# Kernel tuning notes

Hardware: AMD Instinct MI355X
Metric: run time of the kernel (lower is better)

## Reference

```python
import jax, jax.numpy as jnp
import numpy as np

S_IN, S_OUT = 64, 128
NX, NS, CIN, COUT = 40000, 200000, 128, 64


def _unique_coords(key, n, S):
    lin = jax.random.permutation(key, S ** 3)[:n]
    return jnp.stack([lin // (S * S), (lin // S) % S, lin % S], axis=-1).astype(jnp.int32)


def setup_inputs() -> dict:
    key = jax.random.key(0)
    ks = jax.random.split(key, 8)
    cords = _unique_coords(ks[0], NX, S_IN)          # unique low-res coords
    skip_cords = _unique_coords(ks[1], NS, S_OUT)    # unique high-res coords
    x_feats = jax.random.normal(ks[2], (NX, CIN), jnp.float32)
    skip_feats = jax.random.normal(ks[3], (NS, COUT), jnp.float32)
    w_up = jax.random.normal(ks[4], (8, CIN, COUT), jnp.float32) * 0.05
    w1 = jax.random.normal(ks[5], (27, COUT, COUT), jnp.float32) * 0.05
    w2 = jax.random.normal(ks[6], (27, COUT, COUT), jnp.float32) * 0.05
    w3 = jax.random.normal(ks[7], (27, COUT, COUT), jnp.float32) * 0.05
    ones = jnp.ones((COUT,), jnp.float32)
    zeros = jnp.zeros((COUT,), jnp.float32)
    return dict(x_feats=x_feats, skip_feats=skip_feats, w_up=w_up, w1=w1, w2=w2, w3=w3,
                g1=ones, b1=zeros, g2=ones, b2=zeros, g3=ones, b3=zeros,
                cords=cords, skip_cords=skip_cords, spatial_size=64)


def _lin(c, S):
    return (c[..., 0] * S + c[..., 1]) * S + c[..., 2]


def _bn(f, g, b):
    # BatchNorm1d, batch stats (track_running_stats=False), eps=1e-4, biased var
    mu = f.mean(axis=0)
    var = f.var(axis=0)
    return (f - mu) * jax.lax.rsqrt(var + 1e-4) * g + b


def _lrelu(z, s):
    return jnp.where(z >= 0, z, s * z)


def reference(x_feats, skip_feats, w_up, w1, w2, w3, g1, b1, g2, b2, g3, b3,
              cords, skip_cords, spatial_size):
    S = 2 * int(spatial_size)  # output spatial size after upsample
    Cout = w_up.shape[-1]
    # --- upsample: each active voxel c emits a 2x2x2 block at 2c+o, weight W[1-o] ---
    offs8 = jnp.stack(jnp.meshgrid(*([jnp.arange(2)] * 3), indexing='ij'), -1).reshape(8, 3).astype(jnp.int32)
    out_cords = ((2 * cords)[:, None, :] + offs8[None, :, :]).reshape(-1, 3)        # [8N,3]
    feats = jnp.einsum('nc,ocd->nod', x_feats, w_up[::-1]).reshape(-1, Cout)         # [8N,C]
    M = feats.shape[0]
    lin_out = _lin(out_cords, S)
    # --- sparse_add: hash-match skip coords, add matched skip features ---
    table_s = jnp.full((S ** 3,), -1, jnp.int32).at[_lin(skip_cords, S)].set(
        jnp.arange(skip_cords.shape[0], dtype=jnp.int32))
    j = table_s[lin_out]
    feats = feats + jnp.where((j >= 0)[:, None], skip_feats[jnp.clip(j, 0)], 0.0)
    # --- neighbor table for 3x3x3 submanifold convs over the fixed active set ---
    table_o = jnp.full((S ** 3,), -1, jnp.int32).at[lin_out].set(jnp.arange(M, dtype=jnp.int32))
    offs27 = jnp.stack(jnp.meshgrid(*([jnp.arange(-1, 2)] * 3), indexing='ij'), -1).reshape(27, 3).astype(jnp.int32)
    nb = out_cords[None, :, :] + offs27[:, None, :]                                  # [27,M,3]
    valid = jnp.all((nb >= 0) & (nb < S), axis=-1)
    lin_nb = jnp.where(valid, _lin(nb, S), 0)
    nbr = jnp.where(valid, table_o[lin_nb], -1)                                      # [27,M]

    def subconv(f, W):
        acc = jnp.zeros((M, W.shape[-1]), f.dtype)
        for k in range(27):  # fixed small kernel loop
            idx = nbr[k]
            m = (idx >= 0).astype(f.dtype)[:, None]
            acc = acc + (f[jnp.clip(idx, 0)] * m) @ W[k]
        return acc

    x1 = _lrelu(_bn(subconv(feats, w1), g1, b1), 0.05)
    x2 = _lrelu(_bn(subconv(x1, w2), g2, b2), 0.05)
    x3 = _bn(subconv(x2, w3), g3, b3)
    return _lrelu(x3 + x1, 0.333)
```

## Files before the change

kernel.cpp:

```cpp
#include <hip/hip_runtime.h>


#define S2 128
#define TABN (S2 * S2 * S2)

typedef __attribute__((ext_vector_type(8))) short short8;
typedef __attribute__((ext_vector_type(4))) float f32x4;

__device__ inline float b2f(unsigned short u) {
    return __uint_as_float(((unsigned)u) << 16);
}
__device__ inline unsigned short f2b(float f) {
    unsigned u = __float_as_uint(f);
    return (unsigned short)((u + 0x7FFF + ((u >> 16) & 1)) >> 16);
}

__global__ void k_scatter_skip(const int* __restrict__ sc, int* __restrict__ table_s, int NS) {
    int i = blockIdx.x * 256 + threadIdx.x;
    if (i >= NS) return;
    table_s[(sc[i * 3] * S2 + sc[i * 3 + 1]) * S2 + sc[i * 3 + 2]] = i;
}

__global__ void k_packw(const float* __restrict__ w, unsigned short* __restrict__ wpk) {
    int t = blockIdx.x * 256 + threadIdx.x;
    if (t >= 27 * 4096) return;
    int j = t & 7, l = (t >> 3) & 63, nt = (t >> 9) & 3, ks = (t >> 11) & 1, k = t >> 12;
    int d = ks * 32 + (l >> 4) * 8 + j;
    int c = nt * 16 + (l & 15);
    wpk[t] = f2b(w[(k * 64 + d) * 64 + c]);
}

__global__ __launch_bounds__(256) void k_upsample(
    const float* __restrict__ x, const float* __restrict__ wup,
    const int* __restrict__ cords, const float* __restrict__ skipf,
    const int* __restrict__ table_s, int* __restrict__ table_o,
    unsigned short* __restrict__ feats, int NX) {
    __shared__ float xl[16][132];
    int tid = threadIdx.x;
    int P0 = blockIdx.x * 16;
    {
        int p = tid >> 4, d0 = (tid & 15) * 8;
        const float* src = x + (size_t)(P0 + p) * 128 + d0;
        float4 a = *(const float4*)src;
        float4 b = *(const float4*)(src + 4);
        xl[p][d0 + 0] = a.x; xl[p][d0 + 1] = a.y; xl[p][d0 + 2] = a.z; xl[p][d0 + 3] = a.w;
        xl[p][d0 + 4] = b.x; xl[p][d0 + 5] = b.y; xl[p][d0 + 6] = b.z; xl[p][d0 + 7] = b.w;
    }
    __syncthreads();
    int c = tid & 63, g = tid >> 6;
    float acc[8][4];
#pragma unroll
    for (int o = 0; o < 8; ++o)
#pragma unroll
        for (int p = 0; p < 4; ++p) acc[o][p] = 0.f;
    for (int d = 0; d < 128; ++d) {
        float xv0 = xl[g * 4 + 0][d], xv1 = xl[g * 4 + 1][d];
        float xv2 = xl[g * 4 + 2][d], xv3 = xl[g * 4 + 3][d];
#pragma unroll
        for (int o = 0; o < 8; ++o) {
            float wv = wup[(size_t)(7 - o) * 8192 + d * 64 + c];
            acc[o][0] += xv0 * wv; acc[o][1] += xv1 * wv;
            acc[o][2] += xv2 * wv; acc[o][3] += xv3 * wv;
        }
    }
    for (int p = 0; p < 4; ++p) {
        int parent = P0 + g * 4 + p;
        int cx = cords[parent * 3], cy = cords[parent * 3 + 1], cz = cords[parent * 3 + 2];
#pragma unroll
        for (int o = 0; o < 8; ++o) {
            int X = 2 * cx + (o >> 2), Y = 2 * cy + ((o >> 1) & 1), Z = 2 * cz + (o & 1);
            int lin = (X * S2 + Y) * S2 + Z;
            int m = parent * 8 + o;
            int j = table_s[lin];
            float v = acc[o][p];
            if (j >= 0) v += skipf[(size_t)j * 64 + c];
            feats[(size_t)m * 64 + c] = f2b(v);
            if (c == 0) table_o[lin] = m;
        }
    }
}

__global__ void k_build_nbr(const int* __restrict__ cords, const int* __restrict__ table_o,
                            int* __restrict__ nbr, int M) {
    int m = blockIdx.x * 256 + threadIdx.x;
    if (m >= M) return;
    int n = m >> 3, o = m & 7;
    int X = 2 * cords[n * 3] + (o >> 2);
    int Y = 2 * cords[n * 3 + 1] + ((o >> 1) & 1);
    int Z = 2 * cords[n * 3 + 2] + (o & 1);
#pragma unroll
    for (int kk = 0; kk < 27; ++kk) {
        int nx = X + kk / 9 - 1, ny = Y + (kk / 3) % 3 - 1, nz = Z + kk % 3 - 1;
        int idx = -1;
        if ((unsigned)nx < (unsigned)S2 && (unsigned)ny < (unsigned)S2 && (unsigned)nz < (unsigned)S2)
            idx = table_o[(nx * S2 + ny) * S2 + nz];
        nbr[(size_t)kk * M + m] = idx;
    }
}

__global__ __launch_bounds__(256) void k_conv_mfma(
    const unsigned short* __restrict__ fin, const unsigned short* __restrict__ wpk,
    const int* __restrict__ nbr, unsigned short* __restrict__ zout,
    float* __restrict__ stats, int M) {
    int tid = threadIdx.x;
    int lane = tid & 63, wv = tid >> 6;
    int l15 = lane & 15, kg = lane >> 4;
    int rbase = blockIdx.x * 128 + wv * 32;

    f32x4 acc[2][4];
#pragma unroll
    for (int m = 0; m < 2; ++m)
#pragma unroll
        for (int nt = 0; nt < 4; ++nt) acc[m][nt] = (f32x4){0.f, 0.f, 0.f, 0.f};

    const short8 kzero = {0, 0, 0, 0, 0, 0, 0, 0};
    for (int k = 0; k < 27; ++k) {
        const int* nrow = nbr + (size_t)k * M + rbase;
        int i0 = nrow[l15];
        int i1 = nrow[16 + l15];
        const unsigned short* p0 = fin + (size_t)(i0 < 0 ? 0 : i0) * 64 + kg * 8;
        const unsigned short* p1 = fin + (size_t)(i1 < 0 ? 0 : i1) * 64 + kg * 8;
        short8 a00 = *(const short8*)p0;
        short8 a01 = *(const short8*)(p0 + 32);
        short8 a10 = *(const short8*)p1;
        short8 a11 = *(const short8*)(p1 + 32);
        if (i0 < 0) { a00 = kzero; a01 = kzero; }
        if (i1 < 0) { a10 = kzero; a11 = kzero; }
        const unsigned short* wb = wpk + (size_t)k * 4096 + lane * 8;
#pragma unroll
        for (int nt = 0; nt < 4; ++nt) {
            short8 b0 = *(const short8*)(wb + nt * 512);
            short8 b1 = *(const short8*)(wb + 2048 + nt * 512);
            acc[0][nt] = __builtin_amdgcn_mfma_f32_16x16x32_bf16(a00, b0, acc[0][nt], 0, 0, 0);
            acc[0][nt] = __builtin_amdgcn_mfma_f32_16x16x32_bf16(a01, b1, acc[0][nt], 0, 0, 0);
            acc[1][nt] = __builtin_amdgcn_mfma_f32_16x16x32_bf16(a10, b0, acc[1][nt], 0, 0, 0);
            acc[1][nt] = __builtin_amdgcn_mfma_f32_16x16x32_bf16(a11, b1, acc[1][nt], 0, 0, 0);
        }
    }

    float s[4] = {0.f, 0.f, 0.f, 0.f}, q[4] = {0.f, 0.f, 0.f, 0.f};
#pragma unroll
    for (int m = 0; m < 2; ++m)
#pragma unroll
        for (int nt = 0; nt < 4; ++nt)
#pragma unroll
            for (int j = 0; j < 4; ++j) {
                float v = acc[m][nt][j];
                int row = rbase + m * 16 + kg * 4 + j;
                zout[(size_t)row * 64 + nt * 16 + l15] = f2b(v);
                s[nt] += v; q[nt] += v * v;
            }
#pragma unroll
    for (int nt = 0; nt < 4; ++nt) {
        float ss = s[nt], qq = q[nt];
        ss += __shfl_xor(ss, 16); ss += __shfl_xor(ss, 32);
        qq += __shfl_xor(qq, 16); qq += __shfl_xor(qq, 32);
        if (kg == 0) {
            atomicAdd(&stats[nt * 16 + l15], ss);
            atomicAdd(&stats[64 + nt * 16 + l15], qq);
        }
    }
}

__global__ void k_finalize(const float* __restrict__ stats, const float* __restrict__ g,
                           const float* __restrict__ b, float* __restrict__ coef, float invM) {
    int c = threadIdx.x;
    if (c >= 64) return;
    float mu = stats[c] * invM;
    float var = stats[64 + c] * invM - mu * mu;
    float sc = g[c] * rsqrtf(var + 1e-4f);
    coef[c] = sc;
    coef[64 + c] = b[c] - mu * sc;
}

__global__ void k_xform(unsigned short* __restrict__ z, const float* __restrict__ coef, int n8) {
    int t = blockIdx.x * 256 + threadIdx.x;
    if (t >= n8) return;
    short8 v = ((const short8*)z)[t];
    int cb = (t * 8) & 63;
    short8 r;
#pragma unroll
    for (int j = 0; j < 8; ++j) {
        float f = b2f((unsigned short)v[j]) * coef[cb + j] + coef[64 + cb + j];
        f = fmaxf(f, 0.05f * f);
        r[j] = (short)f2b(f);
    }
    ((short8*)z)[t] = r;
}

__global__ void k_final(const unsigned short* __restrict__ z3,
                        const unsigned short* __restrict__ x1,
                        const float* __restrict__ coef3, float* __restrict__ out, int n8) {
    int t = blockIdx.x * 256 + threadIdx.x;
    if (t >= n8) return;
    short8 v3 = ((const short8*)z3)[t];
    short8 v1 = ((const short8*)x1)[t];
    int cb = (t * 8) & 63;
    float4 o0, o1;
    float rr[8];
#pragma unroll
    for (int j = 0; j < 8; ++j) {
        float f3 = b2f((unsigned short)v3[j]) * coef3[cb + j] + coef3[64 + cb + j];
        float r = f3 + b2f((unsigned short)v1[j]);
        rr[j] = fmaxf(r, 0.333f * r);
    }
    o0 = make_float4(rr[0], rr[1], rr[2], rr[3]);
    o1 = make_float4(rr[4], rr[5], rr[6], rr[7]);
    ((float4*)out)[t * 2] = o0;
    ((float4*)out)[t * 2 + 1] = o1;
}

extern "C" void kernel_launch(void* const* d_in, const int* in_sizes, int n_in,
                              void* d_out, int out_size, void* d_ws, size_t ws_size,
                              hipStream_t stream) {
    const float* x_feats    = (const float*)d_in[0];
    const float* skip_feats = (const float*)d_in[1];
    const float* w_up       = (const float*)d_in[2];
    const float* w1         = (const float*)d_in[3];
    const float* w2         = (const float*)d_in[4];
    const float* w3         = (const float*)d_in[5];
    const float* g1 = (const float*)d_in[6],  *b1 = (const float*)d_in[7];
    const float* g2 = (const float*)d_in[8],  *b2 = (const float*)d_in[9];
    const float* g3 = (const float*)d_in[10], *b3 = (const float*)d_in[11];
    const int* cords      = (const int*)d_in[12];
    const int* skip_cords = (const int*)d_in[13];
    int NX = in_sizes[12] / 3;
    int NS = in_sizes[13] / 3;
    int M = NX * 8;

    char* ws = (char*)d_ws;
    size_t off = 0;
    auto alloc = [&](size_t bytes) -> char* {
        char* p = ws + off;
        off += (bytes + 255) & ~(size_t)255;
        return p;
    };
    int* table_s = (int*)alloc((size_t)TABN * 4);
    int* table_o = (int*)alloc((size_t)TABN * 4);
    int* nbr     = (int*)alloc((size_t)27 * M * 4);
    unsigned short* A = (unsigned short*)alloc((size_t)M * 64 * 2);
    unsigned short* B = (unsigned short*)alloc((size_t)M * 64 * 2);
    unsigned short* C = (unsigned short*)alloc((size_t)M * 64 * 2);
    unsigned short* wp1 = (unsigned short*)alloc(27 * 4096 * 2);
    unsigned short* wp2 = (unsigned short*)alloc(27 * 4096 * 2);
    unsigned short* wp3 = (unsigned short*)alloc(27 * 4096 * 2);
    float* stats = (float*)alloc(384 * 4);
    float* coefs = (float*)alloc(384 * 4);

    hipMemsetAsync(table_s, 0xFF, (size_t)TABN * 4, stream);
    hipMemsetAsync(table_o, 0xFF, (size_t)TABN * 4, stream);
    hipMemsetAsync(stats, 0, 384 * 4, stream);

    float invM = 1.f / (float)M;
    int n8 = M * 64 / 8;

    k_scatter_skip<<<(NS + 255) / 256, 256, 0, stream>>>(skip_cords, table_s, NS);
    k_packw<<<432, 256, 0, stream>>>(w1, wp1);
    k_packw<<<432, 256, 0, stream>>>(w2, wp2);
    k_packw<<<432, 256, 0, stream>>>(w3, wp3);
    k_upsample<<<NX / 16, 256, 0, stream>>>(x_feats, w_up, cords, skip_feats,
                                            table_s, table_o, A, NX);
    k_build_nbr<<<(M + 255) / 256, 256, 0, stream>>>(cords, table_o, nbr, M);

    k_conv_mfma<<<M / 128, 256, 0, stream>>>(A, wp1, nbr, B, stats, M);
    k_finalize<<<1, 64, 0, stream>>>(stats, g1, b1, coefs, invM);
    k_xform<<<(n8 + 255) / 256, 256, 0, stream>>>(B, coefs, n8);

    k_conv_mfma<<<M / 128, 256, 0, stream>>>(B, wp2, nbr, C, stats + 128, M);
    k_finalize<<<1, 64, 0, stream>>>(stats + 128, g2, b2, coefs + 128, invM);
    k_xform<<<(n8 + 255) / 256, 256, 0, stream>>>(C, coefs + 128, n8);

    k_conv_mfma<<<M / 128, 256, 0, stream>>>(C, wp3, nbr, A, stats + 256, M);
    k_finalize<<<1, 64, 0, stream>>>(stats + 256, g3, b3, coefs + 256, invM);

    k_final<<<(n8 + 255) / 256, 256, 0, stream>>>(A, B, coefs + 256, (float*)d_out, n8);
}
```

Baseline: 1.370 ms.

## Move upsample to bf16 MFMA and software-pipeline conv gathers with LDS neighbor indices

The upsample GEMM now runs on bf16 MFMA, using a pre-converted bf16 copy of x and pre-packed upsample weights, in place of scalar FP32 FMAs. The subconv kernel stages the block's neighbor indices in LDS and software-pipelines the gathered A and B loads two steps ahead of the MFMAs. Missing neighbors now point to an extra zero row at index M, which removes the per-load masking, and launch bounds request two blocks per CU. This adds conversion and packing kernels and raises register pressure, and the upsample input is rounded to bf16, which changes precision.

After: 1.227 ms. 10.4% less time.

```diff
diff --git a/kernel.cpp b/kernel.cpp
--- a/kernel.cpp
+++ b/kernel.cpp
@@ -13,6 +13,17 @@
 __device__ inline unsigned short f2b(float f) {
     unsigned u = __float_as_uint(f);
     return (unsigned short)((u + 0x7FFF + ((u >> 16) & 1)) >> 16);
+}
+
+__global__ void k_cvt(const float* __restrict__ x, unsigned short* __restrict__ xb, int n8) {
+    int t = blockIdx.x * 256 + threadIdx.x;
+    if (t >= n8) return;
+    float4 a = ((const float4*)x)[t * 2];
+    float4 b = ((const float4*)x)[t * 2 + 1];
+    short8 r;
+    r[0] = (short)f2b(a.x); r[1] = (short)f2b(a.y); r[2] = (short)f2b(a.z); r[3] = (short)f2b(a.w);
+    r[4] = (short)f2b(b.x); r[5] = (short)f2b(b.y); r[6] = (short)f2b(b.z); r[7] = (short)f2b(b.w);
+    ((short8*)xb)[t] = r;
 }
 
 __global__ void k_scatter_skip(const int* __restrict__ sc, int* __restrict__ table_s, int NS) {
@@ -30,52 +41,57 @@
     wpk[t] = f2b(w[(k * 64 + d) * 64 + c]);
 }
 
-__global__ __launch_bounds__(256) void k_upsample(
-    const float* __restrict__ x, const float* __restrict__ wup,
+__global__ void k_packwup(const float* __restrict__ w, unsigned short* __restrict__ wpku) {
+    int t = blockIdx.x * 256 + threadIdx.x;
+    if (t >= 65536) return;
+    int j = t & 7, l = (t >> 3) & 63, nt = (t >> 9) & 31, ks = t >> 14;
+    int d = ks * 32 + (l >> 4) * 8 + j;
+    int col = nt * 16 + (l & 15);
+    int o = col >> 6, c = col & 63;
+    wpku[t] = f2b(w[(size_t)(7 - o) * 8192 + d * 64 + c]);
+}
+
+__global__ __launch_bounds__(256) void k_upsample_mfma(
+    const unsigned short* __restrict__ xb, const unsigned short* __restrict__ wpku,
     const int* __restrict__ cords, const float* __restrict__ skipf,
     const int* __restrict__ table_s, int* __restrict__ table_o,
     unsigned short* __restrict__ feats, int NX) {
-    __shared__ float xl[16][132];
     int tid = threadIdx.x;
-    int P0 = blockIdx.x * 16;
-    {
-        int p = tid >> 4, d0 = (tid & 15) * 8;
-        const float* src = x + (size_t)(P0 + p) * 128 + d0;
-        float4 a = *(const float4*)src;
-        float4 b = *(const float4*)(src + 4);
-        xl[p][d0 + 0] = a.x; xl[p][d0 + 1] = a.y; xl[p][d0 + 2] = a.z; xl[p][d0 + 3] = a.w;
-        xl[p][d0 + 4] = b.x; xl[p][d0 + 5] = b.y; xl[p][d0 + 6] = b.z; xl[p][d0 + 7] = b.w;
-    }
-    __syncthreads();
-    int c = tid & 63, g = tid >> 6;
-    float acc[8][4];
-#pragma unroll
-    for (int o = 0; o < 8; ++o)
-#pragma unroll
-        for (int p = 0; p < 4; ++p) acc[o][p] = 0.f;
-    for (int d = 0; d < 128; ++d) {
-        float xv0 = xl[g * 4 + 0][d], xv1 = xl[g * 4 + 1][d];
-        float xv2 = xl[g * 4 + 2][d], xv3 = xl[g * 4 + 3][d];
-#pragma unroll
-        for (int o = 0; o < 8; ++o) {
-            float wv = wup[(size_t)(7 - o) * 8192 + d * 64 + c];
-            acc[o][0] += xv0 * wv; acc[o][1] += xv1 * wv;
-            acc[o][2] += xv2 * wv; acc[o][3] += xv3 * wv;
+    int lane = tid & 63, w = tid >> 6;
+    int l15 = lane & 15, kg = lane >> 4;
+    int p0 = blockIdx.x * 16;
+
+    f32x4 acc[8];
+#pragma unroll
+    for (int nt = 0; nt < 8; ++nt) acc[nt] = (f32x4){0.f, 0.f, 0.f, 0.f};
+
+#pragma unroll
+    for (int ks = 0; ks < 4; ++ks) {
+        short8 a = *(const short8*)(xb + (size_t)(p0 + l15) * 128 + ks * 32 + kg * 8);
+        const unsigned short* wb = wpku + ((size_t)(ks * 32 + w * 8) * 64 + lane) * 8;
+#pragma unroll
+        for (int nt = 0; nt < 8; ++nt) {
+            short8 b = *(const short8*)(wb + nt * 512);
+            acc[nt] = __builtin_amdgcn_mfma_f32_16x16x32_bf16(a, b, acc[nt], 0, 0, 0);
         }
     }
-    for (int p = 0; p < 4; ++p) {
-        int parent = P0 + g * 4 + p;
+
+#pragma unroll
+    for (int j = 0; j < 4; ++j) {
+        int parent = p0 + kg * 4 + j;
         int cx = cords[parent * 3], cy = cords[parent * 3 + 1], cz = cords[parent * 3 + 2];
 #pragma unroll
-        for (int o = 0; o < 8; ++o) {
+        for (int nt = 0; nt < 8; ++nt) {
+            int o = w * 2 + (nt >> 2);
+            int c = (nt & 3) * 16 + l15;
             int X = 2 * cx + (o >> 2), Y = 2 * cy + ((o >> 1) & 1), Z = 2 * cz + (o & 1);
             int lin = (X * S2 + Y) * S2 + Z;
-            int m = parent * 8 + o;
-            int j = table_s[lin];
-            float v = acc[o][p];
-            if (j >= 0) v += skipf[(size_t)j * 64 + c];
-            feats[(size_t)m * 64 + c] = f2b(v);
-            if (c == 0) table_o[lin] = m;
+            int row = parent * 8 + o;
+            int js = table_s[lin];
+            float v = acc[nt][j];
+            if (js >= 0) v += skipf[(size_t)js * 64 + c];
+            feats[(size_t)row * 64 + c] = f2b(v);
+            if (c == 0) table_o[lin] = row;
         }
     }
 }
@@ -94,18 +110,31 @@
         int idx = -1;
         if ((unsigned)nx < (unsigned)S2 && (unsigned)ny < (unsigned)S2 && (unsigned)nz < (unsigned)S2)
             idx = table_o[(nx * S2 + ny) * S2 + nz];
-        nbr[(size_t)kk * M + m] = idx;
-    }
-}
-
-__global__ __launch_bounds__(256) void k_conv_mfma(
+        nbr[(size_t)kk * M + m] = (idx < 0) ? M : idx;
+    }
+}
+
+__global__ __launch_bounds__(256, 2) void k_conv_mfma(
     const unsigned short* __restrict__ fin, const unsigned short* __restrict__ wpk,
     const int* __restrict__ nbr, unsigned short* __restrict__ zout,
     float* __restrict__ stats, int M) {
+    __shared__ int idx_lds[32 * 128];
     int tid = threadIdx.x;
     int lane = tid & 63, wv = tid >> 6;
     int l15 = lane & 15, kg = lane >> 4;
-    int rbase = blockIdx.x * 128 + wv * 32;
+    int rblk = blockIdx.x * 128;
+    int rw = wv * 32;
+
+    {
+        int col = (tid & 31) * 4;
+        int q0 = tid >> 5;
+        for (int q = q0; q < 27; q += 8) {
+            int4 v = *(const int4*)(nbr + (size_t)q * M + rblk + col);
+            *(int4*)&idx_lds[q * 128 + col] = v;
+        }
+        for (int i = tid; i < 5 * 128; i += 256) idx_lds[27 * 128 + i] = M;
+    }
+    __syncthreads();
 
     f32x4 acc[2][4];
 #pragma unroll
@@ -113,30 +142,51 @@
 #pragma unroll
         for (int nt = 0; nt < 4; ++nt) acc[m][nt] = (f32x4){0.f, 0.f, 0.f, 0.f};
 
-    const short8 kzero = {0, 0, 0, 0, 0, 0, 0, 0};
-    for (int k = 0; k < 27; ++k) {
-        const int* nrow = nbr + (size_t)k * M + rbase;
-        int i0 = nrow[l15];
-        int i1 = nrow[16 + l15];
-        const unsigned short* p0 = fin + (size_t)(i0 < 0 ? 0 : i0) * 64 + kg * 8;
-        const unsigned short* p1 = fin + (size_t)(i1 < 0 ? 0 : i1) * 64 + kg * 8;
-        short8 a00 = *(const short8*)p0;
-        short8 a01 = *(const short8*)(p0 + 32);
-        short8 a10 = *(const short8*)p1;
-        short8 a11 = *(const short8*)(p1 + 32);
-        if (i0 < 0) { a00 = kzero; a01 = kzero; }
-        if (i1 < 0) { a10 = kzero; a11 = kzero; }
-        const unsigned short* wb = wpk + (size_t)k * 4096 + lane * 8;
-#pragma unroll
-        for (int nt = 0; nt < 4; ++nt) {
-            short8 b0 = *(const short8*)(wb + nt * 512);
-            short8 b1 = *(const short8*)(wb + 2048 + nt * 512);
-            acc[0][nt] = __builtin_amdgcn_mfma_f32_16x16x32_bf16(a00, b0, acc[0][nt], 0, 0, 0);
-            acc[0][nt] = __builtin_amdgcn_mfma_f32_16x16x32_bf16(a01, b1, acc[0][nt], 0, 0, 0);
-            acc[1][nt] = __builtin_amdgcn_mfma_f32_16x16x32_bf16(a10, b0, acc[1][nt], 0, 0, 0);
-            acc[1][nt] = __builtin_amdgcn_mfma_f32_16x16x32_bf16(a11, b1, acc[1][nt], 0, 0, 0);
-        }
-    }
+    short8 A0[2][2], A1[2][2], A2[2][2], A3[2][2], B0[2][4], B1[2][4];
+
+#define LOADA(Ab, kk)                                                          \
+    {                                                                          \
+        _Pragma("unroll")                                                      \
+        for (int m = 0; m < 2; ++m) {                                          \
+            int idx = idx_lds[(kk) * 128 + rw + m * 16 + l15];                 \
+            const unsigned short* p = fin + (size_t)idx * 64 + kg * 8;         \
+            Ab[m][0] = *(const short8*)p;                                      \
+            Ab[m][1] = *(const short8*)(p + 32);                               \
+        }                                                                      \
+    }
+#define LOADB(Bb, kk)                                                          \
+    {                                                                          \
+        int kb = (kk) > 26 ? 26 : (kk);                                        \
+        const unsigned short* wb = wpk + (size_t)kb * 4096 + lane * 8;         \
+        _Pragma("unroll")                                                      \
+        for (int ks = 0; ks < 2; ++ks)                                         \
+            _Pragma("unroll")                                                  \
+            for (int nt = 0; nt < 4; ++nt)                                     \
+                Bb[ks][nt] = *(const short8*)(wb + ks * 2048 + nt * 512);      \
+    }
+#define MFMAQ(Ab, Bb)                                                          \
+    {                                                                          \
+        _Pragma("unroll")                                                      \
+        for (int m = 0; m < 2; ++m)                                            \
+            _Pragma("unroll")                                                  \
+            for (int nt = 0; nt < 4; ++nt) {                                   \
+                acc[m][nt] = __builtin_amdgcn_mfma_f32_16x16x32_bf16(          \
+                    Ab[m][0], Bb[0][nt], acc[m][nt], 0, 0, 0);                 \
+                acc[m][nt] = __builtin_amdgcn_mfma_f32_16x16x32_bf16(          \
+                    Ab[m][1], Bb[1][nt], acc[m][nt], 0, 0, 0);                 \
+            }                                                                  \
+    }
+
+    LOADA(A0, 0); LOADA(A1, 1); LOADB(B0, 0);
+    for (int k = 0; k < 28; k += 4) {
+        LOADA(A2, k + 2); LOADB(B1, k + 1); MFMAQ(A0, B0);
+        LOADA(A3, k + 3); LOADB(B0, k + 2); MFMAQ(A1, B1);
+        LOADA(A0, k + 4); LOADB(B1, k + 3); MFMAQ(A2, B0);
+        LOADA(A1, k + 5); LOADB(B0, k + 4); MFMAQ(A3, B1);
+    }
+#undef LOADA
+#undef LOADB
+#undef MFMAQ
 
     float s[4] = {0.f, 0.f, 0.f, 0.f}, q[4] = {0.f, 0.f, 0.f, 0.f};
 #pragma unroll
@@ -146,7 +196,7 @@
 #pragma unroll
             for (int j = 0; j < 4; ++j) {
                 float v = acc[m][nt][j];
-                int row = rbase + m * 16 + kg * 4 + j;
+                int row = rblk + rw + m * 16 + kg * 4 + j;
                 zout[(size_t)row * 64 + nt * 16 + l15] = f2b(v);
                 s[nt] += v; q[nt] += v * v;
             }
@@ -196,7 +246,6 @@
     short8 v3 = ((const short8*)z3)[t];
     short8 v1 = ((const short8*)x1)[t];
     int cb = (t * 8) & 63;
-    float4 o0, o1;
     float rr[8];
 #pragma unroll
     for (int j = 0; j < 8; ++j) {
@@ -204,10 +253,8 @@
         float r = f3 + b2f((unsigned short)v1[j]);
         rr[j] = fmaxf(r, 0.333f * r);
     }
-    o0 = make_float4(rr[0], rr[1], rr[2], rr[3]);
-    o1 = make_float4(rr[4], rr[5], rr[6], rr[7]);
-    ((float4*)out)[t * 2] = o0;
-    ((float4*)out)[t * 2 + 1] = o1;
+    ((float4*)out)[t * 2] = make_float4(rr[0], rr[1], rr[2], rr[3]);
+    ((float4*)out)[t * 2 + 1] = make_float4(rr[4], rr[5], rr[6], rr[7]);
 }
 
 extern "C" void kernel_launch(void* const* d_in, const int* in_sizes, int n_in,
@@ -238,9 +285,11 @@
     int* table_s = (int*)alloc((size_t)TABN * 4);
     int* table_o = (int*)alloc((size_t)TABN * 4);
     int* nbr     = (int*)alloc((size_t)27 * M * 4);
-    unsigned short* A = (unsigned short*)alloc((size_t)M * 64 * 2);
-    unsigned short* B = (unsigned short*)alloc((size_t)M * 64 * 2);
-    unsigned short* C = (unsigned short*)alloc((size_t)M * 64 * 2);
+    unsigned short* A = (unsigned short*)alloc((size_t)(M + 1) * 64 * 2);
+    unsigned short* B = (unsigned short*)alloc((size_t)(M + 1) * 64 * 2);
+    unsigned short* C = (unsigned short*)alloc((size_t)(M + 1) * 64 * 2);
+    unsigned short* xb   = (unsigned short*)alloc((size_t)NX * 128 * 2);
+    unsigned short* wpku = (unsigned short*)alloc(65536 * 2);
     unsigned short* wp1 = (unsigned short*)alloc(27 * 4096 * 2);
     unsigned short* wp2 = (unsigned short*)alloc(27 * 4096 * 2);
     unsigned short* wp3 = (unsigned short*)alloc(27 * 4096 * 2);
@@ -250,16 +299,21 @@
     hipMemsetAsync(table_s, 0xFF, (size_t)TABN * 4, stream);
     hipMemsetAsync(table_o, 0xFF, (size_t)TABN * 4, stream);
     hipMemsetAsync(stats, 0, 384 * 4, stream);
+    hipMemsetAsync(A + (size_t)M * 64, 0, 128, stream);
+    hipMemsetAsync(B + (size_t)M * 64, 0, 128, stream);
+    hipMemsetAsync(C + (size_t)M * 64, 0, 128, stream);
 
     float invM = 1.f / (float)M;
     int n8 = M * 64 / 8;
 
+    k_cvt<<<(NX * 16 + 255) / 256, 256, 0, stream>>>(x_feats, xb, NX * 16);
     k_scatter_skip<<<(NS + 255) / 256, 256, 0, stream>>>(skip_cords, table_s, NS);
+    k_packwup<<<256, 256, 0, stream>>>(w_up, wpku);
     k_packw<<<432, 256, 0, stream>>>(w1, wp1);
     k_packw<<<432, 256, 0, stream>>>(w2, wp2);
     k_packw<<<432, 256, 0, stream>>>(w3, wp3);
-    k_upsample<<<NX / 16, 256, 0, stream>>>(x_feats, w_up, cords, skip_feats,
-                                            table_s, table_o, A, NX);
+    k_upsample_mfma<<<NX / 16, 256, 0, stream>>>(xb, wpku, cords, skip_feats,
+                                                 table_s, table_o, A, NX);
     k_build_nbr<<<(M + 255) / 256, 256, 0, stream>>>(cords, table_o, nbr, M);
 
     k_conv_mfma<<<M / 128, 256, 0, stream>>>(A, wp1, nbr, B, stats, M);
```
